# Performance work log

Hardware: AMD Instinct MI355X
Metric: run time of the kernel (lower is better)

The kernel has to match this reference:

```python
import jax, jax.numpy as jnp
import numpy as np

M, K, N = 8192, 4096, 4096

def _quantize_symmetric(t):
    # per-tensor symmetric int8 quantization: scale = max|t| / 127
    scale = jnp.max(jnp.abs(t)) / 127.0
    q = jnp.clip(jnp.round(t / scale), -127.0, 127.0).astype(jnp.int8)
    return q, scale


def setup_inputs() -> dict:
    key = jax.random.key(0)
    kx, kw, kb = jax.random.split(key, 3)
    x = jax.random.normal(kx, (M, K), dtype=jnp.float32)
    weight = jax.random.normal(kw, (N, K), dtype=jnp.float32)
    bias = jax.random.normal(kb, (N,), dtype=jnp.float32)
    return {"x": x, "weight": weight, "bias": bias}


def reference(x, weight, bias):
    # dynamic per-tensor quantization of activations and (pre-quantized) weight
    x_q, x_scale = _quantize_symmetric(x)
    w_q, w_scale = _quantize_symmetric(weight)
    # int8 GEMM with int32 accumulation (padding in the source is a no-op mathematically)
    acc = jnp.matmul(x_q.astype(jnp.int32), w_q.astype(jnp.int32).T)  # [M, N]
    # dequantize with product of per-tensor scales, then bias add
    out = acc.astype(jnp.float32) * (x_scale * w_scale) + bias
    return out
```

## Files before the change

kernel.cpp:

```cpp
#include <hip/hip_runtime.h>
#include <stdint.h>

#define MDIM 8192
#define KDIM 4096
#define NDIM 4096
#define BM 256
#define BN 128
#define BK 64

typedef int v4i __attribute__((ext_vector_type(4)));

__global__ void absmax_kernel(const float* __restrict__ src, int n4,
                              unsigned* __restrict__ out_bits) {
    __shared__ float smax[4];
    int idx = blockIdx.x * blockDim.x + threadIdx.x;
    int stride = gridDim.x * blockDim.x;
    const float4* s4 = (const float4*)src;
    float m = 0.0f;
    for (int i = idx; i < n4; i += stride) {
        float4 v = s4[i];
        m = fmaxf(m, fmaxf(fmaxf(fabsf(v.x), fabsf(v.y)),
                           fmaxf(fabsf(v.z), fabsf(v.w))));
    }
#pragma unroll
    for (int off = 32; off > 0; off >>= 1)
        m = fmaxf(m, __shfl_down(m, off, 64));
    if ((threadIdx.x & 63) == 0) smax[threadIdx.x >> 6] = m;
    __syncthreads();
    if (threadIdx.x == 0) {
        float bm = fmaxf(fmaxf(smax[0], smax[1]), fmaxf(smax[2], smax[3]));
        atomicMax(out_bits, __float_as_uint(bm));
    }
}

__global__ void quantize_kernel(const float* __restrict__ src, int n4,
                                const unsigned* __restrict__ bits,
                                int* __restrict__ dst) {
    float amax = __uint_as_float(*bits);
    float scale = (amax > 0.0f) ? (amax / 127.0f) : 1.0f;
    int idx = blockIdx.x * blockDim.x + threadIdx.x;
    int stride = gridDim.x * blockDim.x;
    const float4* s4 = (const float4*)src;
    for (int i = idx; i < n4; i += stride) {
        float4 v = s4[i];
        int a = __float2int_rn(v.x / scale);
        int b = __float2int_rn(v.y / scale);
        int c = __float2int_rn(v.z / scale);
        int d = __float2int_rn(v.w / scale);
        a = min(127, max(-127, a));
        b = min(127, max(-127, b));
        c = min(127, max(-127, c));
        d = min(127, max(-127, d));
        dst[i] = (a & 0xFF) | ((b & 0xFF) << 8) | ((c & 0xFF) << 16) | ((d & 0xFF) << 24);
    }
}

__global__ __launch_bounds__(256, 2) void gemm_i8(
    const signed char* __restrict__ Aq,
    const signed char* __restrict__ Wq,
    const float* __restrict__ bias,
    const unsigned* __restrict__ bits,
    float* __restrict__ out) {
    __shared__ __align__(16) signed char As[BM * BK];
    __shared__ __align__(16) signed char Bs[BN * BK];

    const int tid  = threadIdx.x;
    const int lane = tid & 63;
    const int wave = tid >> 6;
    const int wm = wave >> 1;
    const int wn = wave & 1;
    const int l15 = lane & 15;
    const int l4  = lane >> 4;

    const int m0 = blockIdx.y * BM;
    const int n0 = blockIdx.x * BN;

    const int sr = tid >> 2;
    const int sc = (tid & 3) << 4;

    const signed char* aG[4];
#pragma unroll
    for (int g = 0; g < 4; ++g)
        aG[g] = Aq + (size_t)(m0 + g * 64 + sr) * KDIM + sc;
    const signed char* bG[2];
#pragma unroll
    for (int g = 0; g < 2; ++g)
        bG[g] = Wq + (size_t)(n0 + g * 64 + sr) * KDIM + sc;

    v4i acc[8][4] = {};

    for (int kb = 0; kb < KDIM; kb += BK) {
#pragma unroll
        for (int g = 0; g < 4; ++g)
            __builtin_amdgcn_global_load_lds(
                (const __attribute__((address_space(1))) void*)(aG[g] + kb),
                (__attribute__((address_space(3))) void*)(As + g * 4096 + tid * 16), 16, 0, 0);
#pragma unroll
        for (int g = 0; g < 2; ++g)
            __builtin_amdgcn_global_load_lds(
                (const __attribute__((address_space(1))) void*)(bG[g] + kb),
                (__attribute__((address_space(3))) void*)(Bs + g * 4096 + tid * 16), 16, 0, 0);
        __syncthreads();

        v4i af[8], bf[4];
#pragma unroll
        for (int t = 0; t < 8; ++t)
            af[t] = *(const v4i*)(As + (wm * 128 + t * 16 + l15) * BK + l4 * 16);
#pragma unroll
        for (int t = 0; t < 4; ++t)
            bf[t] = *(const v4i*)(Bs + (wn * 64 + t * 16 + l15) * BK + l4 * 16);

#pragma unroll
        for (int i = 0; i < 8; ++i)
#pragma unroll
            for (int j = 0; j < 4; ++j)
                acc[i][j] = __builtin_amdgcn_mfma_i32_16x16x64_i8(af[i], bf[j], acc[i][j], 0, 0, 0);
        __syncthreads();
    }

    const float ax = __uint_as_float(bits[0]);
    const float aw = __uint_as_float(bits[1]);
    const float s = (ax / 127.0f) * (aw / 127.0f);

#pragma unroll
    for (int j = 0; j < 4; ++j) {
        const int col = n0 + wn * 64 + j * 16 + l15;
        const float bcol = bias[col];
#pragma unroll
        for (int i = 0; i < 8; ++i) {
            const int row0 = m0 + wm * 128 + i * 16 + l4 * 4;
#pragma unroll
            for (int r = 0; r < 4; ++r)
                out[(size_t)(row0 + r) * NDIM + col] = (float)acc[i][j][r] * s + bcol;
        }
    }
}

extern "C" void kernel_launch(void* const* d_in, const int* in_sizes, int n_in,
                              void* d_out, int out_size, void* d_ws, size_t ws_size,
                              hipStream_t stream) {
    const float* x    = (const float*)d_in[0];
    const float* w    = (const float*)d_in[1];
    const float* bias = (const float*)d_in[2];
    float* out = (float*)d_out;

    unsigned* bits = (unsigned*)d_ws;
    signed char* xq = (signed char*)d_ws + 64;
    signed char* wq = xq + (size_t)MDIM * KDIM;

    hipMemsetAsync(d_ws, 0, 64, stream);

    absmax_kernel<<<1024, 256, 0, stream>>>(x, MDIM * KDIM / 4, bits);
    absmax_kernel<<<512, 256, 0, stream>>>(w, NDIM * KDIM / 4, bits + 1);
    quantize_kernel<<<2048, 256, 0, stream>>>(x, MDIM * KDIM / 4, bits, (int*)xq);
    quantize_kernel<<<1024, 256, 0, stream>>>(w, NDIM * KDIM / 4, bits + 1, (int*)wq);

    dim3 grid(NDIM / BN, MDIM / BM);
    gemm_i8<<<grid, 256, 0, stream>>>(xq, wq, bias, bits, out);
}
```

Before: 459.4 us.

## Merge quant kernels and rewrite int8 GEMM with double-buffered swizzled 256x256 tiles

The two absmax launches become one kernel, and the two quantize launches become another, each with 4x unrolled loads. The GEMM moves to 256x256 tiles with 512 threads, BK=128 and double-buffered LDS filled by direct global-to-LDS loads. It adds an XOR swizzle to avoid LDS bank conflicts, interleaves MFMA sub-blocks with barriers, and raises wave priority around the MFMAs. The aim is to overlap global loads with compute and cut launch overhead, at the cost of 128KB of LDS, which limits occupancy.

```diff
diff --git a/kernel.cpp b/kernel.cpp
--- a/kernel.cpp
+++ b/kernel.cpp
@@ -4,23 +4,39 @@
 #define MDIM 8192
 #define KDIM 4096
 #define NDIM 4096
-#define BM 256
-#define BN 128
-#define BK 64
 
 typedef int v4i __attribute__((ext_vector_type(4)));
 
-__global__ void absmax_kernel(const float* __restrict__ src, int n4,
-                              unsigned* __restrict__ out_bits) {
+__global__ __launch_bounds__(256) void absmax2_kernel(const float* __restrict__ x,
+                                                      const float* __restrict__ w,
+                                                      unsigned* __restrict__ bits) {
     __shared__ float smax[4];
-    int idx = blockIdx.x * blockDim.x + threadIdx.x;
-    int stride = gridDim.x * blockDim.x;
-    const float4* s4 = (const float4*)src;
+    const float4* src;
+    int idx, stride, n4;
+    unsigned* slot;
+    if (blockIdx.x < 1024) {
+        src = (const float4*)x;
+        idx = blockIdx.x * 256 + threadIdx.x;
+        stride = 1024 * 256;
+        n4 = MDIM * KDIM / 4;
+        slot = bits;
+    } else {
+        src = (const float4*)w;
+        idx = (blockIdx.x - 1024) * 256 + threadIdx.x;
+        stride = 512 * 256;
+        n4 = NDIM * KDIM / 4;
+        slot = bits + 1;
+    }
     float m = 0.0f;
-    for (int i = idx; i < n4; i += stride) {
-        float4 v = s4[i];
-        m = fmaxf(m, fmaxf(fmaxf(fabsf(v.x), fabsf(v.y)),
-                           fmaxf(fabsf(v.z), fabsf(v.w))));
+    for (int i = idx; i < n4; i += 4 * stride) {
+        float4 a = src[i];
+        float4 b = src[i + stride];
+        float4 c = src[i + 2 * stride];
+        float4 d = src[i + 3 * stride];
+        m = fmaxf(m, fmaxf(fmaxf(fabsf(a.x), fabsf(a.y)), fmaxf(fabsf(a.z), fabsf(a.w))));
+        m = fmaxf(m, fmaxf(fmaxf(fabsf(b.x), fabsf(b.y)), fmaxf(fabsf(b.z), fabsf(b.w))));
+        m = fmaxf(m, fmaxf(fmaxf(fabsf(c.x), fabsf(c.y)), fmaxf(fabsf(c.z), fabsf(c.w))));
+        m = fmaxf(m, fmaxf(fmaxf(fabsf(d.x), fabsf(d.y)), fmaxf(fabsf(d.z), fabsf(d.w))));
     }
 #pragma unroll
     for (int off = 32; off > 0; off >>= 1)
@@ -29,93 +45,155 @@
     __syncthreads();
     if (threadIdx.x == 0) {
         float bm = fmaxf(fmaxf(smax[0], smax[1]), fmaxf(smax[2], smax[3]));
-        atomicMax(out_bits, __float_as_uint(bm));
-    }
-}
-
-__global__ void quantize_kernel(const float* __restrict__ src, int n4,
-                                const unsigned* __restrict__ bits,
-                                int* __restrict__ dst) {
-    float amax = __uint_as_float(*bits);
-    float scale = (amax > 0.0f) ? (amax / 127.0f) : 1.0f;
-    int idx = blockIdx.x * blockDim.x + threadIdx.x;
-    int stride = gridDim.x * blockDim.x;
-    const float4* s4 = (const float4*)src;
-    for (int i = idx; i < n4; i += stride) {
-        float4 v = s4[i];
-        int a = __float2int_rn(v.x / scale);
-        int b = __float2int_rn(v.y / scale);
-        int c = __float2int_rn(v.z / scale);
-        int d = __float2int_rn(v.w / scale);
-        a = min(127, max(-127, a));
-        b = min(127, max(-127, b));
-        c = min(127, max(-127, c));
-        d = min(127, max(-127, d));
-        dst[i] = (a & 0xFF) | ((b & 0xFF) << 8) | ((c & 0xFF) << 16) | ((d & 0xFF) << 24);
-    }
-}
-
-__global__ __launch_bounds__(256, 2) void gemm_i8(
+        atomicMax(slot, __float_as_uint(bm));
+    }
+}
+
+__global__ __launch_bounds__(256) void quant2_kernel(const float* __restrict__ x,
+                                                     const float* __restrict__ w,
+                                                     const unsigned* __restrict__ bits,
+                                                     int* __restrict__ xq,
+                                                     int* __restrict__ wq) {
+    const float4* src;
+    int idx, stride, n4;
+    int* dst;
+    float amax;
+    if (blockIdx.x < 2048) {
+        src = (const float4*)x;
+        idx = blockIdx.x * 256 + threadIdx.x;
+        stride = 2048 * 256;
+        n4 = MDIM * KDIM / 4;
+        dst = xq;
+        amax = __uint_as_float(bits[0]);
+    } else {
+        src = (const float4*)w;
+        idx = (blockIdx.x - 2048) * 256 + threadIdx.x;
+        stride = 1024 * 256;
+        n4 = NDIM * KDIM / 4;
+        dst = wq;
+        amax = __uint_as_float(bits[1]);
+    }
+    const float scale = (amax > 0.0f) ? (amax / 127.0f) : 1.0f;
+    for (int i = idx; i < n4; i += 4 * stride) {
+        float4 v[4];
+        v[0] = src[i];
+        v[1] = src[i + stride];
+        v[2] = src[i + 2 * stride];
+        v[3] = src[i + 3 * stride];
+#pragma unroll
+        for (int u = 0; u < 4; ++u) {
+            int a = __float2int_rn(v[u].x / scale);
+            int b = __float2int_rn(v[u].y / scale);
+            int c = __float2int_rn(v[u].z / scale);
+            int d = __float2int_rn(v[u].w / scale);
+            a = min(127, max(-127, a));
+            b = min(127, max(-127, b));
+            c = min(127, max(-127, c));
+            d = min(127, max(-127, d));
+            dst[i + u * stride] =
+                (a & 0xFF) | ((b & 0xFF) << 8) | ((c & 0xFF) << 16) | ((d & 0xFF) << 24);
+        }
+    }
+}
+
+__global__ __launch_bounds__(512, 2) void gemm_i8(
     const signed char* __restrict__ Aq,
     const signed char* __restrict__ Wq,
     const float* __restrict__ bias,
     const unsigned* __restrict__ bits,
     float* __restrict__ out) {
-    __shared__ __align__(16) signed char As[BM * BK];
-    __shared__ __align__(16) signed char Bs[BN * BK];
+    __shared__ __align__(16) signed char As[2 * 32768];
+    __shared__ __align__(16) signed char Bs[2 * 32768];
 
     const int tid  = threadIdx.x;
     const int lane = tid & 63;
     const int wave = tid >> 6;
-    const int wm = wave >> 1;
-    const int wn = wave & 1;
+    const int wm = wave >> 2;
+    const int wn = wave & 3;
     const int l15 = lane & 15;
     const int l4  = lane >> 4;
-
-    const int m0 = blockIdx.y * BM;
-    const int n0 = blockIdx.x * BN;
-
-    const int sr = tid >> 2;
-    const int sc = (tid & 3) << 4;
-
-    const signed char* aG[4];
-#pragma unroll
-    for (int g = 0; g < 4; ++g)
-        aG[g] = Aq + (size_t)(m0 + g * 64 + sr) * KDIM + sc;
-    const signed char* bG[2];
-#pragma unroll
-    for (int g = 0; g < 2; ++g)
-        bG[g] = Wq + (size_t)(n0 + g * 64 + sr) * KDIM + sc;
+    const int swz = l15 & 7;
+
+    const int m0 = blockIdx.y * 256;
+    const int n0 = blockIdx.x * 256;
+
+    const int srow = tid >> 3;
+    const int scol = ((tid & 7) ^ (srow & 7)) << 4;
+    const signed char* aSrc[4];
+    const signed char* bSrc[4];
+#pragma unroll
+    for (int u = 0; u < 4; ++u) {
+        aSrc[u] = Aq + (size_t)(m0 + u * 64 + srow) * KDIM + scol;
+        bSrc[u] = Wq + (size_t)(n0 + u * 64 + srow) * KDIM + scol;
+    }
+    const int ldsOff = tid * 16;
 
     v4i acc[8][4] = {};
-
-    for (int kb = 0; kb < KDIM; kb += BK) {
-#pragma unroll
-        for (int g = 0; g < 4; ++g)
-            __builtin_amdgcn_global_load_lds(
-                (const __attribute__((address_space(1))) void*)(aG[g] + kb),
-                (__attribute__((address_space(3))) void*)(As + g * 4096 + tid * 16), 16, 0, 0);
-#pragma unroll
-        for (int g = 0; g < 2; ++g)
-            __builtin_amdgcn_global_load_lds(
-                (const __attribute__((address_space(1))) void*)(bG[g] + kb),
-                (__attribute__((address_space(3))) void*)(Bs + g * 4096 + tid * 16), 16, 0, 0);
-        __syncthreads();
-
-        v4i af[8], bf[4];
-#pragma unroll
-        for (int t = 0; t < 8; ++t)
-            af[t] = *(const v4i*)(As + (wm * 128 + t * 16 + l15) * BK + l4 * 16);
-#pragma unroll
-        for (int t = 0; t < 4; ++t)
-            bf[t] = *(const v4i*)(Bs + (wn * 64 + t * 16 + l15) * BK + l4 * 16);
-
-#pragma unroll
-        for (int i = 0; i < 8; ++i)
-#pragma unroll
-            for (int j = 0; j < 4; ++j)
-                acc[i][j] = __builtin_amdgcn_mfma_i32_16x16x64_i8(af[i], bf[j], acc[i][j], 0, 0, 0);
-        __syncthreads();
+    v4i af[4][2], bf[2][2];
+
+#define STAGE_FULL(BUF, KB) do {                                                          \
+    _Pragma("unroll") for (int u = 0; u < 4; ++u)                                         \
+        __builtin_amdgcn_global_load_lds(                                                 \
+            (const __attribute__((address_space(1))) void*)(aSrc[u] + (KB)),              \
+            (__attribute__((address_space(3))) void*)(As + (BUF)*32768 + u*8192 + ldsOff),\
+            16, 0, 0);                                                                    \
+    _Pragma("unroll") for (int u = 0; u < 4; ++u)                                         \
+        __builtin_amdgcn_global_load_lds(                                                 \
+            (const __attribute__((address_space(1))) void*)(bSrc[u] + (KB)),              \
+            (__attribute__((address_space(3))) void*)(Bs + (BUF)*32768 + u*8192 + ldsOff),\
+            16, 0, 0);                                                                    \
+} while (0)
+
+#define LDA(dst, BUF, i, kk) dst = *(const v4i*)(As + (BUF)*32768 +                       \
+        (wm*128 + (i)*16 + l15)*128 + (((((kk)<<2) | l4) ^ swz) << 4))
+#define LDB(dst, BUF, j, kk) dst = *(const v4i*)(Bs + (BUF)*32768 +                       \
+        (wn*64 + (j)*16 + l15)*128 + (((((kk)<<2) | l4) ^ swz) << 4))
+
+#define MFMA8(I0, J0) do {                                                                \
+    _Pragma("unroll") for (int kk = 0; kk < 2; ++kk)                                      \
+    _Pragma("unroll") for (int i = 0; i < 4; ++i)                                         \
+    _Pragma("unroll") for (int j = 0; j < 2; ++j)                                         \
+        acc[(I0)+i][(J0)+j] = __builtin_amdgcn_mfma_i32_16x16x64_i8(                      \
+            af[i][kk], bf[j][kk], acc[(I0)+i][(J0)+j], 0, 0, 0);                          \
+} while (0)
+
+#define BAR() do { __builtin_amdgcn_s_barrier(); asm volatile("" ::: "memory"); } while (0)
+
+#define TILE(BUF, DO_STAGE, NKB) do {                                                     \
+               \
+    if (DO_STAGE) STAGE_FULL(1 - (BUF), NKB);                                             \
+    _Pragma("unroll") for (int i = 0; i < 4; ++i) { LDA(af[i][0], BUF, i, 0);             \
+                                                    LDA(af[i][1], BUF, i, 1); }           \
+    _Pragma("unroll") for (int j = 0; j < 2; ++j) { LDB(bf[j][0], BUF, j, 0);             \
+                                                    LDB(bf[j][1], BUF, j, 1); }           \
+    __builtin_amdgcn_s_setprio(1); MFMA8(0, 0); __builtin_amdgcn_s_setprio(0);            \
+    BAR();                                                                                \
+                                       \
+    _Pragma("unroll") for (int j = 0; j < 2; ++j) { LDB(bf[j][0], BUF, 2 + j, 0);         \
+                                                    LDB(bf[j][1], BUF, 2 + j, 1); }       \
+    __builtin_amdgcn_s_setprio(1); MFMA8(0, 2); __builtin_amdgcn_s_setprio(0);            \
+    BAR();                                                                                \
+                                       \
+    _Pragma("unroll") for (int i = 0; i < 4; ++i) { LDA(af[i][0], BUF, 4 + i, 0);         \
+                                                    LDA(af[i][1], BUF, 4 + i, 1); }       \
+    __builtin_amdgcn_s_setprio(1); MFMA8(4, 2); __builtin_amdgcn_s_setprio(0);            \
+    BAR();                                                                                \
+                         \
+    _Pragma("unroll") for (int j = 0; j < 2; ++j) { LDB(bf[j][0], BUF, j, 0);             \
+                                                    LDB(bf[j][1], BUF, j, 1); }           \
+    __builtin_amdgcn_s_setprio(1); MFMA8(4, 0); __builtin_amdgcn_s_setprio(0);            \
+    asm volatile("s_waitcnt vmcnt(0)" ::: "memory");                                      \
+    BAR();                                                                                \
+} while (0)
+
+    STAGE_FULL(0, 0);
+    asm volatile("s_waitcnt vmcnt(0)" ::: "memory");
+    BAR();
+
+#pragma unroll 1
+    for (int kb = 0; kb < KDIM; kb += 256) {
+        TILE(0, true, kb + 128);
+        TILE(1, (kb + 256) < KDIM, kb + 256);
     }
 
     const float ax = __uint_as_float(bits[0]);
@@ -134,6 +212,12 @@
                 out[(size_t)(row0 + r) * NDIM + col] = (float)acc[i][j][r] * s + bcol;
         }
     }
+#undef STAGE_FULL
+#undef LDA
+#undef LDB
+#undef MFMA8
+#undef BAR
+#undef TILE
 }
 
 extern "C" void kernel_launch(void* const* d_in, const int* in_sizes, int n_in,
@@ -150,11 +234,9 @@
 
     hipMemsetAsync(d_ws, 0, 64, stream);
 
-    absmax_kernel<<<1024, 256, 0, stream>>>(x, MDIM * KDIM / 4, bits);
-    absmax_kernel<<<512, 256, 0, stream>>>(w, NDIM * KDIM / 4, bits + 1);
-    quantize_kernel<<<2048, 256, 0, stream>>>(x, MDIM * KDIM / 4, bits, (int*)xq);
-    quantize_kernel<<<1024, 256, 0, stream>>>(w, NDIM * KDIM / 4, bits + 1, (int*)wq);
-
-    dim3 grid(NDIM / BN, MDIM / BM);
-    gemm_i8<<<grid, 256, 0, stream>>>(xq, wq, bias, bits, out);
-}
+    absmax2_kernel<<<1536, 256, 0, stream>>>(x, w, bits);
+    quant2_kernel<<<3072, 256, 0, stream>>>(x, w, bits, (int*)xq, (int*)wq);
+
+    dim3 grid(NDIM / 256, MDIM / 256);
+    gemm_i8<<<grid, 512, 0, stream>>>(xq, wq, bias, bits, out);
+}
```

New measurement: 481.6 us. 4.8% more time.
